# Optimization experiments

Hardware: AMD Instinct MI355X
Metric: run time of the kernel (lower is better)

## Reference

```python
import jax, jax.numpy as jnp
import numpy as np

N, E, G, H, NF, EF, GF, L = 204800, 600000, 3200, 128, 16, 5, 8, 6
EPS = 1e-5


def setup_inputs() -> dict:
    key = jax.random.key(0)
    ks = jax.random.split(key, 24)
    s = 0.05
    inp = {
        'x': jax.random.normal(ks[0], (N, NF), jnp.float32),
        'edge_index': jax.random.randint(ks[1], (2, E), 0, N, jnp.int32),
        'edge_attr': jax.random.normal(ks[2], (E, EF), jnp.float32),
        'global_features': jax.random.normal(ks[3], (G, GF), jnp.float32),
        'batch': (jnp.arange(N, dtype=jnp.int32) // (N // G)),
        'node_w': jax.random.normal(ks[4], (NF, H), jnp.float32) * s,
        'node_b': jnp.zeros((H,), jnp.float32),
        'edge_w': jax.random.normal(ks[5], (EF, H), jnp.float32) * s,
        'edge_b': jnp.zeros((H,), jnp.float32),
        'rel_w': jax.random.normal(ks[6], (L, H, H), jnp.float32) * s,
        'rel_b': jnp.zeros((L, H), jnp.float32),
        'root_w': jax.random.normal(ks[7], (L, H, H), jnp.float32) * s,
        'bn_gamma': jnp.ones((L, H), jnp.float32),
        'bn_beta': jnp.zeros((L, H), jnp.float32),
        'gate_w1': jax.random.normal(ks[8], (H, H), jnp.float32) * s,
        'gate_b1': jnp.zeros((H,), jnp.float32),
        'gate_w2': jax.random.normal(ks[9], (H, 1), jnp.float32) * s,
        'gate_b2': jnp.zeros((1,), jnp.float32),
        'gf_w': jax.random.normal(ks[10], (GF, H), jnp.float32) * s,
        'gf_b': jnp.zeros((H,), jnp.float32),
        'gi_w': jax.random.normal(ks[11], (2 * H, H), jnp.float32) * s,
        'gi_b': jnp.zeros((H,), jnp.float32),
    }
    return inp


def reference(x, edge_index, edge_attr, global_features, batch,
              node_w, node_b, edge_w, edge_b,
              rel_w, rel_b, root_w, bn_gamma, bn_beta,
              gate_w1, gate_b1, gate_w2, gate_b2,
              gf_w, gf_b, gi_w, gi_b):
    n = x.shape[0]
    src, dst = edge_index[0], edge_index[1]
    h = x @ node_w + node_b                       # [N,H]
    ea = edge_attr @ edge_w + edge_b              # [E,H]
    for i in range(L):
        identity = h
        msg = h[src] * ea                         # [E,H] gather + edge weighting
        agg = jax.ops.segment_sum(msg, dst, num_segments=n)  # scatter-add
        h2 = agg @ rel_w[i] + rel_b[i] + h @ root_w[i]        # GraphConv
        mean = jnp.mean(h2, axis=0)
        var = jnp.mean(jnp.square(h2 - mean), axis=0)         # biased (BN train)
        h2 = (h2 - mean) * jax.lax.rsqrt(var + EPS) * bn_gamma[i] + bn_beta[i]
        h = jax.nn.relu(h2 + identity)
    # GlobalAttention: segment softmax over gate scores, weighted sum of h
    gate = (jax.nn.relu(h @ gate_w1 + gate_b1) @ gate_w2 + gate_b2)[:, 0]  # [N]
    m = jax.ops.segment_max(gate, batch, num_segments=G)
    e = jnp.exp(gate - m[batch])
    ssum = jax.ops.segment_sum(e, batch, num_segments=G)
    alpha = e / ssum[batch]
    pooled = jax.ops.segment_sum(alpha[:, None] * h, batch, num_segments=G)  # [G,H]
    gf = global_features @ gf_w + gf_b
    global_embedding = jnp.concatenate([pooled, gf], axis=1) @ gi_w + gi_b
    return (h, global_embedding)
```

## Files before the change

kernel.cpp:

```cpp
#include <hip/hip_runtime.h>
#include <math.h>

#define N_NODES 204800
#define N_EDGES 600000
#define N_GRAPH 3200
#define H 128
#define NF 16
#define EF 5
#define GF 8
#define LAYERS 6
#define SEG 64
#define EPSV 1e-5f
#define NB_SCAN 800
#define NBLK 3200

typedef __attribute__((ext_vector_type(8))) short bf16x8;
typedef __attribute__((ext_vector_type(4))) float f32x4;

__device__ inline float bf2f(unsigned int u) {
    return __builtin_bit_cast(float, u << 16);
}
__device__ inline unsigned short f2bf(float f) {
    unsigned int u = __builtin_bit_cast(unsigned int, f);
    u += 0x7fffu + ((u >> 16) & 1u);
    return (unsigned short)(u >> 16);
}
__device__ inline float uif(unsigned int u) { return __builtin_bit_cast(float, u); }

__global__ __launch_bounds__(256) void k_init_h(
    const float* __restrict__ x, const float* __restrict__ node_w,
    const float* __restrict__ node_b, unsigned short* __restrict__ hb)
{
    int idx = blockIdx.x * 256 + threadIdx.x;
    int n = idx >> 5, c0 = (idx & 31) * 4;
    float4 a = *(const float4*)(node_b + c0);
    const float* xr = x + n * NF;
#pragma unroll
    for (int k = 0; k < NF; ++k) {
        float xv = xr[k];
        float4 wv = *(const float4*)(node_w + k * H + c0);
        a.x += xv * wv.x; a.y += xv * wv.y; a.z += xv * wv.z; a.w += xv * wv.w;
    }
    unsigned int p0 = (unsigned int)f2bf(a.x) | ((unsigned int)f2bf(a.y) << 16);
    unsigned int p1 = (unsigned int)f2bf(a.z) | ((unsigned int)f2bf(a.w) << 16);
    *(uint2*)(hb + (size_t)n * H + c0) = make_uint2(p0, p1);
}

__global__ __launch_bounds__(64) void k_wpack(
    const float* __restrict__ relw, const float* __restrict__ rootw,
    unsigned short* __restrict__ wp)
{
    int bid = blockIdx.x;
    int i = bid >> 6, f = bid & 63;
    int nb = f >> 3, ks = f & 7;
    int l = threadIdx.x;
    const float* src = (ks < 4) ? (relw + (size_t)i * H * H) : (rootw + (size_t)i * H * H);
    int ksl = ks & 3;
    int col = nb * 16 + (l & 15);
    int kbase = ksl * 32 + (l >> 4) * 8;
    unsigned short tmp[8];
#pragma unroll
    for (int m = 0; m < 8; ++m)
        tmp[m] = f2bf(src[(size_t)(kbase + m) * H + col]);
    *(uint4*)(wp + ((size_t)bid * 64 + l) * 8) = *(uint4*)tmp;
}

__global__ __launch_bounds__(64) void k_wpack_gate(
    const float* __restrict__ gw1, unsigned short* __restrict__ gwp)
{
    int bid = blockIdx.x;
    int nb = bid >> 2, ks = bid & 3;
    int l = threadIdx.x;
    int col = nb * 16 + (l & 15);
    int kbase = ks * 32 + (l >> 4) * 8;
    unsigned short tmp[8];
#pragma unroll
    for (int m = 0; m < 8; ++m)
        tmp[m] = f2bf(gw1[(size_t)(kbase + m) * H + col]);
    *(uint4*)(gwp + ((size_t)bid * 64 + l) * 8) = *(uint4*)tmp;
}

__global__ __launch_bounds__(256) void k_deg(const int* __restrict__ ei, int* __restrict__ deg)
{
    int e = blockIdx.x * 256 + threadIdx.x;
    if (e < N_EDGES) atomicAdd(&deg[ei[N_EDGES + e]], 1);
}

__global__ __launch_bounds__(256) void k_scan1(
    const int* __restrict__ deg, int* __restrict__ rowtmp, int* __restrict__ bsum)
{
    __shared__ int sh[256];
    int t = threadIdx.x;
    int i = blockIdx.x * 256 + t;
    int v = deg[i];
    sh[t] = v;
    __syncthreads();
    for (int off = 1; off < 256; off <<= 1) {
        int a = (t >= off) ? sh[t - off] : 0;
        __syncthreads();
        sh[t] += a;
        __syncthreads();
    }
    rowtmp[i] = sh[t] - v;
    if (t == 255) bsum[blockIdx.x] = sh[255];
}

__global__ void k_scan2(int* __restrict__ bsum, int* __restrict__ boff)
{
    __shared__ int sh[256];
    __shared__ int carry;
    int t = threadIdx.x;
    if (t == 0) carry = 0;
    __syncthreads();
    for (int base = 0; base < NB_SCAN; base += 256) {
        int i = base + t;
        int v = (i < NB_SCAN) ? bsum[i] : 0;
        sh[t] = v;
        __syncthreads();
        for (int off = 1; off < 256; off <<= 1) {
            int a = (t >= off) ? sh[t - off] : 0;
            __syncthreads();
            sh[t] += a;
            __syncthreads();
        }
        if (i < NB_SCAN) boff[i] = carry + sh[t] - v;
        __syncthreads();
        if (t == 0) carry += sh[255];
        __syncthreads();
    }
}

__global__ __launch_bounds__(256) void k_scan3(
    const int* __restrict__ rowtmp, const int* __restrict__ boff,
    int* __restrict__ rowptr, int* __restrict__ cursor)
{
    int i = blockIdx.x * 256 + threadIdx.x;
    int r = rowtmp[i] + boff[blockIdx.x];
    rowptr[i] = r;
    cursor[i] = r;
    if (i == 0) rowptr[N_NODES] = N_EDGES;
}

__global__ __launch_bounds__(256) void k_scatter(
    const int* __restrict__ ei, const float* __restrict__ eattr,
    int* __restrict__ cursor, uint4* __restrict__ recs)
{
    int e = blockIdx.x * 256 + threadIdx.x;
    if (e >= N_EDGES) return;
    int d = ei[N_EDGES + e];
    const float* ar = eattr + (size_t)e * EF;
    float c0 = ar[0], c1 = ar[1], c2 = ar[2], c3 = ar[3], c4 = ar[4];
    int pos = atomicAdd(&cursor[d], 1);
    uint4 q0, q1;
    q0.x = (unsigned int)ei[e];
    q0.y = __builtin_bit_cast(unsigned int, c0);
    q0.z = __builtin_bit_cast(unsigned int, c1);
    q0.w = __builtin_bit_cast(unsigned int, c2);
    q1.x = __builtin_bit_cast(unsigned int, c3);
    q1.y = __builtin_bit_cast(unsigned int, c4);
    q1.z = 0; q1.w = 0;
    recs[2 * (size_t)pos]     = q0;
    recs[2 * (size_t)pos + 1] = q1;
}

#define EDGE_ONE(q0, q1, A0, A1)                                               \
    {                                                                          \
        unsigned int hv = *(const unsigned int*)(hb + (size_t)(int)(q0).x * H + 2 * l); \
        float ea0 = eb2.x, ea1 = eb2.y;                                        \
        float c0 = uif((q0).y), c1 = uif((q0).z), c2 = uif((q0).w);            \
        float c3 = uif((q1).x), c4 = uif((q1).y);                              \
        ea0 += c0 * ew2[0].x + c1 * ew2[1].x + c2 * ew2[2].x + c3 * ew2[3].x + c4 * ew2[4].x; \
        ea1 += c0 * ew2[0].y + c1 * ew2[1].y + c2 * ew2[2].y + c3 * ew2[3].y + c4 * ew2[4].y; \
        A0 += bf2f(hv & 0xffffu) * ea0;                                        \
        A1 += bf2f(hv >> 16) * ea1;                                            \
    }

__global__ __launch_bounds__(256) void k_agg(
    const int* __restrict__ rowptr, const uint4* __restrict__ recs,
    const float* __restrict__ edge_w, const float* __restrict__ edge_b,
    const unsigned short* __restrict__ hb, unsigned short* __restrict__ aggb)
{
    int w = threadIdx.x >> 6, l = threadIdx.x & 63;
    int n = blockIdx.x * 8 + w * 2;
    float2 ew2[EF];
#pragma unroll
    for (int k = 0; k < EF; ++k) ew2[k] = ((const float2*)(edge_w + k * H))[l];
    float2 eb2 = ((const float2*)edge_b)[l];

    int jA = rowptr[n], eA = rowptr[n + 1];
    int jB = eA,        eB = rowptr[n + 2];
    float a0 = 0.f, a1 = 0.f, b0 = 0.f, b1 = 0.f;

    while (jA + 2 <= eA && jB + 2 <= eB) {
        uint4 qa0 = recs[2 * jA],     qa1 = recs[2 * jA + 1];
        uint4 qb0 = recs[2 * jA + 2], qb1 = recs[2 * jA + 3];
        uint4 qc0 = recs[2 * jB],     qc1 = recs[2 * jB + 1];
        uint4 qd0 = recs[2 * jB + 2], qd1 = recs[2 * jB + 3];
        EDGE_ONE(qa0, qa1, a0, a1);
        EDGE_ONE(qb0, qb1, a0, a1);
        EDGE_ONE(qc0, qc1, b0, b1);
        EDGE_ONE(qd0, qd1, b0, b1);
        jA += 2; jB += 2;
    }
    while (jA + 2 <= eA) {
        uint4 qa0 = recs[2 * jA],     qa1 = recs[2 * jA + 1];
        uint4 qb0 = recs[2 * jA + 2], qb1 = recs[2 * jA + 3];
        EDGE_ONE(qa0, qa1, a0, a1);
        EDGE_ONE(qb0, qb1, a0, a1);
        jA += 2;
    }
    if (jA < eA) {
        uint4 qa0 = recs[2 * jA], qa1 = recs[2 * jA + 1];
        EDGE_ONE(qa0, qa1, a0, a1);
    }
    while (jB + 2 <= eB) {
        uint4 qc0 = recs[2 * jB],     qc1 = recs[2 * jB + 1];
        uint4 qd0 = recs[2 * jB + 2], qd1 = recs[2 * jB + 3];
        EDGE_ONE(qc0, qc1, b0, b1);
        EDGE_ONE(qd0, qd1, b0, b1);
        jB += 2;
    }
    if (jB < eB) {
        uint4 qc0 = recs[2 * jB], qc1 = recs[2 * jB + 1];
        EDGE_ONE(qc0, qc1, b0, b1);
    }

    unsigned int pka = (unsigned int)f2bf(a0) | ((unsigned int)f2bf(a1) << 16);
    unsigned int pkb = (unsigned int)f2bf(b0) | ((unsigned int)f2bf(b1) << 16);
    *(unsigned int*)(aggb + (size_t)n * H + 2 * l)       = pka;
    *(unsigned int*)(aggb + (size_t)(n + 1) * H + 2 * l) = pkb;
}

__global__ __launch_bounds__(256) void k_gemm_mfma(
    const unsigned short* __restrict__ aggb,
    const unsigned short* __restrict__ hb,
    const unsigned short* __restrict__ wp,
    const float* __restrict__ relb,
    unsigned short* __restrict__ h2b,
    float* __restrict__ pbuf)
{
    __shared__ unsigned short smA[64 * 128];
    __shared__ unsigned short smH[64 * 128];
    int tid = threadIdx.x;
    int w = tid >> 6, l = tid & 63;
    int bid = blockIdx.x;
    int n0 = bid * 64;
    int lr = l & 15, hi = l >> 4;

    const char* aggp = (const char*)(aggb + (size_t)n0 * H);
    const char* hbp  = (const char*)(hb  + (size_t)n0 * H);
    char* sA = (char*)smA;
    char* sH = (char*)smH;
#pragma unroll
    for (int i = 0; i < 4; ++i) {
        int o = (i * 256 + tid) * 16;
        int row = o >> 8;
        int col = o & 255;
        int scol = col ^ ((row & 7) << 4);
        uint4 va = *(const uint4*)(aggp + o);
        uint4 vh = *(const uint4*)(hbp + o);
        *(uint4*)(sA + row * 256 + scol) = va;
        *(uint4*)(sH + row * 256 + scol) = vh;
    }
    __syncthreads();

    f32x4 acc[4][2];
#pragma unroll
    for (int rb = 0; rb < 4; ++rb) {
        acc[rb][0] = (f32x4){0.f, 0.f, 0.f, 0.f};
        acc[rb][1] = (f32x4){0.f, 0.f, 0.f, 0.f};
    }

    const bf16x8* wv = (const bf16x8*)wp;
#pragma unroll
    for (int ks = 0; ks < 4; ++ks) {
        bf16x8 b0 = wv[((2 * w + 0) * 8 + ks) * 64 + l];
        bf16x8 b1 = wv[((2 * w + 1) * 8 + ks) * 64 + l];
#pragma unroll
        for (int rb = 0; rb < 4; ++rb) {
            int r = rb * 16 + lr;
            int bc = (ks * 64 + hi * 16) ^ ((r & 7) << 4);
            bf16x8 a = *(const bf16x8*)(sA + r * 256 + bc);
            acc[rb][0] = __builtin_amdgcn_mfma_f32_16x16x32_bf16(a, b0, acc[rb][0], 0, 0, 0);
            acc[rb][1] = __builtin_amdgcn_mfma_f32_16x16x32_bf16(a, b1, acc[rb][1], 0, 0, 0);
        }
    }
#pragma unroll
    for (int ks = 0; ks < 4; ++ks) {
        bf16x8 b0 = wv[((2 * w + 0) * 8 + 4 + ks) * 64 + l];
        bf16x8 b1 = wv[((2 * w + 1) * 8 + 4 + ks) * 64 + l];
#pragma unroll
        for (int rb = 0; rb < 4; ++rb) {
            int r = rb * 16 + lr;
            int bc = (ks * 64 + hi * 16) ^ ((r & 7) << 4);
            bf16x8 a = *(const bf16x8*)(sH + r * 256 + bc);
            acc[rb][0] = __builtin_amdgcn_mfma_f32_16x16x32_bf16(a, b0, acc[rb][0], 0, 0, 0);
            acc[rb][1] = __builtin_amdgcn_mfma_f32_16x16x32_bf16(a, b1, acc[rb][1], 0, 0, 0);
        }
    }

#pragma unroll
    for (int nbl = 0; nbl < 2; ++nbl) {
        int col = w * 32 + nbl * 16 + lr;
        float bs = relb[col];
        float csum = 0.f, csq = 0.f;
#pragma unroll
        for (int rb = 0; rb < 4; ++rb) {
#pragma unroll
            for (int jj = 0; jj < 4; ++jj) {
                float v = acc[rb][nbl][jj] + bs;
                h2b[(size_t)(n0 + rb * 16 + hi * 4 + jj) * H + col] = f2bf(v);
                csum += v; csq += v * v;
            }
        }
        csum += __shfl_xor(csum, 16); csum += __shfl_xor(csum, 32);
        csq  += __shfl_xor(csq, 16);  csq  += __shfl_xor(csq, 32);
        if (hi == 0) {
            pbuf[(size_t)col * NBLK + bid]         = csum;
            pbuf[(size_t)(128 + col) * NBLK + bid] = csq;
        }
    }
}

__global__ __launch_bounds__(256) void k_red(
    const float* __restrict__ pbuf, const float* __restrict__ gamma,
    const float* __restrict__ beta, float* __restrict__ stats)
{
    __shared__ float sh[8];
    int c = blockIdx.x;
    int t = threadIdx.x;
    float s = 0.f, q = 0.f;
    const float* ps = pbuf + (size_t)c * NBLK;
    const float* pq = pbuf + (size_t)(128 + c) * NBLK;
    for (int i = t; i < NBLK; i += 256) { s += ps[i]; q += pq[i]; }
#pragma unroll
    for (int off = 32; off >= 1; off >>= 1) {
        s += __shfl_xor(s, off);
        q += __shfl_xor(q, off);
    }
    if ((t & 63) == 0) { sh[t >> 6] = s; sh[4 + (t >> 6)] = q; }
    __syncthreads();
    if (t == 0) {
        float S = sh[0] + sh[1] + sh[2] + sh[3];
        float Q = sh[4] + sh[5] + sh[6] + sh[7];
        float mean = S / (float)N_NODES;
        float var = fmaxf(Q / (float)N_NODES - mean * mean, 0.f);
        float scale = gamma[c] * rsqrtf(var + EPSV);
        stats[c] = scale;
        stats[128 + c] = beta[c] - mean * scale;
    }
}

template<bool LAST>
__global__ __launch_bounds__(256) void k_bn_apply(
    const unsigned short* __restrict__ h2b, const float* __restrict__ stats,
    unsigned short* __restrict__ hb, float* __restrict__ h)
{
    __shared__ float ssc[H], ssh[H];
    int tid = threadIdx.x;
    if (tid < H) {
        ssc[tid] = stats[tid];
        ssh[tid] = stats[128 + tid];
    }
    __syncthreads();
    size_t base = ((size_t)blockIdx.x * 256 + tid) * 8;
    int c = (int)(base & 127);
    uint4 hv2 = *(const uint4*)(h2b + base);
    uint4 hvp = *(const uint4*)(hb + base);
    unsigned int u2[4] = {hv2.x, hv2.y, hv2.z, hv2.w};
    unsigned int up[4] = {hvp.x, hvp.y, hvp.z, hvp.w};
    float o[8];
#pragma unroll
    for (int k = 0; k < 4; ++k) {
        float vlo = bf2f(u2[k] & 0xffffu), vhi = bf2f(u2[k] >> 16);
        float plo = bf2f(up[k] & 0xffffu), phi = bf2f(up[k] >> 16);
        o[2 * k]     = fmaxf(vlo * ssc[c + 2 * k]     + ssh[c + 2 * k]     + plo, 0.f);
        o[2 * k + 1] = fmaxf(vhi * ssc[c + 2 * k + 1] + ssh[c + 2 * k + 1] + phi, 0.f);
    }
    uint4 pk;
    pk.x = (unsigned int)f2bf(o[0]) | ((unsigned int)f2bf(o[1]) << 16);
    pk.y = (unsigned int)f2bf(o[2]) | ((unsigned int)f2bf(o[3]) << 16);
    pk.z = (unsigned int)f2bf(o[4]) | ((unsigned int)f2bf(o[5]) << 16);
    pk.w = (unsigned int)f2bf(o[6]) | ((unsigned int)f2bf(o[7]) << 16);
    *(uint4*)(hb + base) = pk;
    if (LAST) {
        *(float4*)(h + base)     = make_float4(o[0], o[1], o[2], o[3]);
        *(float4*)(h + base + 4) = make_float4(o[4], o[5], o[6], o[7]);
    }
}

__global__ __launch_bounds__(256) void k_gate_pool(
    const unsigned short* __restrict__ hb, const float* __restrict__ h,
    const unsigned short* __restrict__ gwp,
    const float* __restrict__ b1, const float* __restrict__ w2,
    const float* __restrict__ b2, float* __restrict__ pooled)
{
    __shared__ float Red[256];
    __shared__ float al[64];
    int tid = threadIdx.x;
    int w = tid >> 6, l = tid & 63;
    int lr = l & 15, hi = l >> 4;
    int g = blockIdx.x;
    int n0 = g * SEG;

    f32x4 acc[4][2];
#pragma unroll
    for (int rb = 0; rb < 4; ++rb) {
        acc[rb][0] = (f32x4){0.f, 0.f, 0.f, 0.f};
        acc[rb][1] = (f32x4){0.f, 0.f, 0.f, 0.f};
    }
    const bf16x8* wv = (const bf16x8*)gwp;
#pragma unroll
    for (int ks = 0; ks < 4; ++ks) {
        bf16x8 bb0 = wv[((2 * w + 0) * 4 + ks) * 64 + l];
        bf16x8 bb1 = wv[((2 * w + 1) * 4 + ks) * 64 + l];
#pragma unroll
        for (int rb = 0; rb < 4; ++rb) {
            bf16x8 a = *(const bf16x8*)(hb + (size_t)(n0 + rb * 16 + lr) * H + ks * 32 + hi * 8);
            acc[rb][0] = __builtin_amdgcn_mfma_f32_16x16x32_bf16(a, bb0, acc[rb][0], 0, 0, 0);
            acc[rb][1] = __builtin_amdgcn_mfma_f32_16x16x32_bf16(a, bb1, acc[rb][1], 0, 0, 0);
        }
    }
    int col0 = w * 32 + lr, col1 = w * 32 + 16 + lr;
    float b10 = b1[col0], b11 = b1[col1];
    float w20 = w2[col0], w21 = w2[col1];
    float p[4][4];
#pragma unroll
    for (int rb = 0; rb < 4; ++rb)
#pragma unroll
        for (int jj = 0; jj < 4; ++jj) {
            float v0 = fmaxf(acc[rb][0][jj] + b10, 0.f);
            float v1 = fmaxf(acc[rb][1][jj] + b11, 0.f);
            float s = v0 * w20 + v1 * w21;
            s += __shfl_xor(s, 1); s += __shfl_xor(s, 2);
            s += __shfl_xor(s, 4); s += __shfl_xor(s, 8);
            p[rb][jj] = s;
        }
    if (lr == 0) {
#pragma unroll
        for (int rb = 0; rb < 4; ++rb)
#pragma unroll
            for (int jj = 0; jj < 4; ++jj)
                Red[w * 64 + rb * 16 + hi * 4 + jj] = p[rb][jj];
    }
    __syncthreads();
    if (tid < 64) {
        float gt = Red[tid] + Red[64 + tid] + Red[128 + tid] + Red[192 + tid] + b2[0];
        float m = gt;
#pragma unroll
        for (int off = 32; off >= 1; off >>= 1) m = fmaxf(m, __shfl_xor(m, off));
        float e = expf(gt - m);
        float s = e;
#pragma unroll
        for (int off = 32; off >= 1; off >>= 1) s += __shfl_xor(s, off);
        al[tid] = e / s;
    }
    __syncthreads();
    int c = tid & 127, half = tid >> 7;
    float pp = 0.f;
    const float* hbase = h + (size_t)n0 * H;
    for (int j = half * 32; j < half * 32 + 32; ++j)
        pp += al[j] * hbase[(size_t)j * H + c];
    Red[tid] = pp;
    __syncthreads();
    if (tid < 128) pooled[(size_t)g * H + tid] = Red[tid] + Red[128 + tid];
}

__global__ __launch_bounds__(128) void k_final(
    const float* __restrict__ pooled, const float* __restrict__ gfeat,
    const float* __restrict__ gf_w, const float* __restrict__ gf_b,
    const float* __restrict__ gi_w, const float* __restrict__ gi_b,
    float* __restrict__ out)
{
    int g = blockIdx.x, c = threadIdx.x;
    __shared__ float prow[H], gfs[H];
    prow[c] = pooled[(size_t)g * H + c];
    float gv = gf_b[c];
    const float* gr = gfeat + (size_t)g * GF;
#pragma unroll
    for (int k = 0; k < GF; ++k) gv += gr[k] * gf_w[k * H + c];
    gfs[c] = gv;
    __syncthreads();
    float acc = gi_b[c];
    for (int k = 0; k < H; ++k) acc += prow[k] * gi_w[k * H + c];
    for (int k = 0; k < H; ++k) acc += gfs[k] * gi_w[(H + k) * H + c];
    out[(size_t)N_NODES * H + (size_t)g * H + c] = acc;
}

extern "C" void kernel_launch(void* const* d_in, const int* in_sizes, int n_in,
                              void* d_out, int out_size, void* d_ws, size_t ws_size,
                              hipStream_t stream)
{
    const float* x       = (const float*)d_in[0];
    const int*   ei      = (const int*)d_in[1];
    const float* eattr   = (const float*)d_in[2];
    const float* gfeat   = (const float*)d_in[3];
    const float* node_w  = (const float*)d_in[5];
    const float* node_b  = (const float*)d_in[6];
    const float* edge_w  = (const float*)d_in[7];
    const float* edge_b  = (const float*)d_in[8];
    const float* rel_w   = (const float*)d_in[9];
    const float* rel_b   = (const float*)d_in[10];
    const float* root_w  = (const float*)d_in[11];
    const float* bn_g    = (const float*)d_in[12];
    const float* bn_b    = (const float*)d_in[13];
    const float* gate_w1 = (const float*)d_in[14];
    const float* gate_b1 = (const float*)d_in[15];
    const float* gate_w2 = (const float*)d_in[16];
    const float* gate_b2 = (const float*)d_in[17];
    const float* gf_w    = (const float*)d_in[18];
    const float* gf_b    = (const float*)d_in[19];
    const float* gi_w    = (const float*)d_in[20];
    const float* gi_b    = (const float*)d_in[21];

    float* h   = (float*)d_out;
    float* out = (float*)d_out;

    char* wsb = (char*)d_ws;
    size_t off = 0;
    auto take = [&](size_t bytes) -> char* {
        char* r = wsb + off;
        off = (off + bytes + 63) & ~(size_t)63;
        return r;
    };
    unsigned short* h2b  = (unsigned short*)take((size_t)N_NODES * H * 2);
    unsigned short* hb   = (unsigned short*)take((size_t)N_NODES * H * 2);
    unsigned short* aggb = (unsigned short*)take((size_t)N_NODES * H * 2);
    unsigned short* wpck = (unsigned short*)take((size_t)LAYERS * 32768 * 2);
    unsigned short* gwp  = (unsigned short*)take((size_t)16384 * 2);
    float* pbuf   = (float*)take((size_t)256 * NBLK * 4);
    float* stats  = (float*)take((size_t)256 * 4);
    float* pooled = (float*)take((size_t)N_GRAPH * H * 4);
    int*   deg    = (int*)take((size_t)N_NODES * 4);
    int*   rowptr = (int*)take((size_t)(N_NODES + 1) * 4);
    int*   cursor = (int*)take((size_t)N_NODES * 4);
    int*   bsum   = (int*)take((size_t)NB_SCAN * 4);
    int*   boff   = (int*)take((size_t)NB_SCAN * 4);
    uint4* recs   = (uint4*)take((size_t)N_EDGES * 32);
    int*   rowtmp = cursor;

    hipMemsetAsync(deg, 0, N_NODES * sizeof(int), stream);
    k_deg<<<(N_EDGES + 255) / 256, 256, 0, stream>>>(ei, deg);
    k_scan1<<<NB_SCAN, 256, 0, stream>>>(deg, rowtmp, bsum);
    k_scan2<<<1, 256, 0, stream>>>(bsum, boff);
    k_scan3<<<NB_SCAN, 256, 0, stream>>>(rowtmp, boff, rowptr, cursor);
    k_scatter<<<(N_EDGES + 255) / 256, 256, 0, stream>>>(ei, eattr, cursor, recs);
    k_wpack<<<LAYERS * 64, 64, 0, stream>>>(rel_w, root_w, wpck);
    k_wpack_gate<<<32, 64, 0, stream>>>(gate_w1, gwp);

    k_init_h<<<N_NODES * 32 / 256, 256, 0, stream>>>(x, node_w, node_b, hb);

    for (int i = 0; i < LAYERS; ++i) {
        k_agg<<<N_NODES / 8, 256, 0, stream>>>(rowptr, recs, edge_w, edge_b, hb, aggb);
        k_gemm_mfma<<<NBLK, 256, 0, stream>>>(
            aggb, hb, wpck + (size_t)i * 32768, rel_b + (size_t)i * H,
            h2b, pbuf);
        k_red<<<128, 256, 0, stream>>>(pbuf, bn_g + (size_t)i * H, bn_b + (size_t)i * H, stats);
        if (i < LAYERS - 1)
            k_bn_apply<false><<<N_NODES * H / 8 / 256, 256, 0, stream>>>(h2b, stats, hb, h);
        else
            k_bn_apply<true><<<N_NODES * H / 8 / 256, 256, 0, stream>>>(h2b, stats, hb, h);
    }

    k_gate_pool<<<N_GRAPH, 256, 0, stream>>>(hb, h, gwp, gate_b1, gate_w2, gate_b2, pooled);
    k_final<<<N_GRAPH, H, 0, stream>>>(pooled, gfeat, gf_w, gf_b, gi_w, gi_b, out);
}
```

Before: 1.044 ms.

## Interleave four nodes per wave in aggregation with software-prefetched edge records

The aggregation kernel now has each wave process four destination nodes in lockstep instead of two. Each node's edge stream is masked so they share one loop bounded by the maximum degree, and the next edge records are loaded while the current ones are accumulated. The aim is more independent gathers in flight per wave to hide memory latency. The cost is wasted lanes of work when node degrees differ, plus extra dummy record loads at index 0. Initial embedding now has each thread compute 8 output columns with vectorized x loads and 16-byte stores.

```diff
diff --git a/kernel.cpp b/kernel.cpp
--- a/kernel.cpp
+++ b/kernel.cpp
@@ -32,18 +32,27 @@
     const float* __restrict__ node_b, unsigned short* __restrict__ hb)
 {
     int idx = blockIdx.x * 256 + threadIdx.x;
-    int n = idx >> 5, c0 = (idx & 31) * 4;
-    float4 a = *(const float4*)(node_b + c0);
-    const float* xr = x + n * NF;
+    int n = idx >> 4, c0 = (idx & 15) * 8;
+    const float4* xr = (const float4*)(x + (size_t)n * NF);
+    float4 x0 = xr[0], x1 = xr[1], x2 = xr[2], x3 = xr[3];
+    float xa[16] = {x0.x, x0.y, x0.z, x0.w, x1.x, x1.y, x1.z, x1.w,
+                    x2.x, x2.y, x2.z, x2.w, x3.x, x3.y, x3.z, x3.w};
+    float4 a0 = *(const float4*)(node_b + c0);
+    float4 a1 = *(const float4*)(node_b + c0 + 4);
 #pragma unroll
     for (int k = 0; k < NF; ++k) {
-        float xv = xr[k];
-        float4 wv = *(const float4*)(node_w + k * H + c0);
-        a.x += xv * wv.x; a.y += xv * wv.y; a.z += xv * wv.z; a.w += xv * wv.w;
-    }
-    unsigned int p0 = (unsigned int)f2bf(a.x) | ((unsigned int)f2bf(a.y) << 16);
-    unsigned int p1 = (unsigned int)f2bf(a.z) | ((unsigned int)f2bf(a.w) << 16);
-    *(uint2*)(hb + (size_t)n * H + c0) = make_uint2(p0, p1);
+        float xv = xa[k];
+        float4 w0 = *(const float4*)(node_w + k * H + c0);
+        float4 w1 = *(const float4*)(node_w + k * H + c0 + 4);
+        a0.x += xv * w0.x; a0.y += xv * w0.y; a0.z += xv * w0.z; a0.w += xv * w0.w;
+        a1.x += xv * w1.x; a1.y += xv * w1.y; a1.z += xv * w1.z; a1.w += xv * w1.w;
+    }
+    uint4 pk;
+    pk.x = (unsigned int)f2bf(a0.x) | ((unsigned int)f2bf(a0.y) << 16);
+    pk.y = (unsigned int)f2bf(a0.z) | ((unsigned int)f2bf(a0.w) << 16);
+    pk.z = (unsigned int)f2bf(a1.x) | ((unsigned int)f2bf(a1.y) << 16);
+    pk.w = (unsigned int)f2bf(a1.z) | ((unsigned int)f2bf(a1.w) << 16);
+    *(uint4*)(hb + (size_t)n * H + c0) = pk;
 }
 
 __global__ __launch_bounds__(64) void k_wpack(
@@ -163,16 +172,17 @@
     recs[2 * (size_t)pos + 1] = q1;
 }
 
-#define EDGE_ONE(q0, q1, A0, A1)                                               \
+#define EDGE_C(q0, q1, hv, vmask, A0, A1)                                      \
     {                                                                          \
-        unsigned int hv = *(const unsigned int*)(hb + (size_t)(int)(q0).x * H + 2 * l); \
         float ea0 = eb2.x, ea1 = eb2.y;                                        \
         float c0 = uif((q0).y), c1 = uif((q0).z), c2 = uif((q0).w);            \
         float c3 = uif((q1).x), c4 = uif((q1).y);                              \
         ea0 += c0 * ew2[0].x + c1 * ew2[1].x + c2 * ew2[2].x + c3 * ew2[3].x + c4 * ew2[4].x; \
         ea1 += c0 * ew2[0].y + c1 * ew2[1].y + c2 * ew2[2].y + c3 * ew2[3].y + c4 * ew2[4].y; \
-        A0 += bf2f(hv & 0xffffu) * ea0;                                        \
-        A1 += bf2f(hv >> 16) * ea1;                                            \
+        ea0 = (vmask) ? ea0 : 0.f;                                             \
+        ea1 = (vmask) ? ea1 : 0.f;                                             \
+        A0 += bf2f((hv) & 0xffffu) * ea0;                                      \
+        A1 += bf2f((hv) >> 16) * ea1;                                          \
     }
 
 __global__ __launch_bounds__(256) void k_agg(
@@ -181,54 +191,61 @@
     const unsigned short* __restrict__ hb, unsigned short* __restrict__ aggb)
 {
     int w = threadIdx.x >> 6, l = threadIdx.x & 63;
-    int n = blockIdx.x * 8 + w * 2;
+    int n = blockIdx.x * 16 + w * 4;
     float2 ew2[EF];
 #pragma unroll
     for (int k = 0; k < EF; ++k) ew2[k] = ((const float2*)(edge_w + k * H))[l];
     float2 eb2 = ((const float2*)edge_b)[l];
 
-    int jA = rowptr[n], eA = rowptr[n + 1];
-    int jB = eA,        eB = rowptr[n + 2];
-    float a0 = 0.f, a1 = 0.f, b0 = 0.f, b1 = 0.f;
-
-    while (jA + 2 <= eA && jB + 2 <= eB) {
-        uint4 qa0 = recs[2 * jA],     qa1 = recs[2 * jA + 1];
-        uint4 qb0 = recs[2 * jA + 2], qb1 = recs[2 * jA + 3];
-        uint4 qc0 = recs[2 * jB],     qc1 = recs[2 * jB + 1];
-        uint4 qd0 = recs[2 * jB + 2], qd1 = recs[2 * jB + 3];
-        EDGE_ONE(qa0, qa1, a0, a1);
-        EDGE_ONE(qb0, qb1, a0, a1);
-        EDGE_ONE(qc0, qc1, b0, b1);
-        EDGE_ONE(qd0, qd1, b0, b1);
-        jA += 2; jB += 2;
-    }
-    while (jA + 2 <= eA) {
-        uint4 qa0 = recs[2 * jA],     qa1 = recs[2 * jA + 1];
-        uint4 qb0 = recs[2 * jA + 2], qb1 = recs[2 * jA + 3];
-        EDGE_ONE(qa0, qa1, a0, a1);
-        EDGE_ONE(qb0, qb1, a0, a1);
-        jA += 2;
-    }
-    if (jA < eA) {
-        uint4 qa0 = recs[2 * jA], qa1 = recs[2 * jA + 1];
-        EDGE_ONE(qa0, qa1, a0, a1);
-    }
-    while (jB + 2 <= eB) {
-        uint4 qc0 = recs[2 * jB],     qc1 = recs[2 * jB + 1];
-        uint4 qd0 = recs[2 * jB + 2], qd1 = recs[2 * jB + 3];
-        EDGE_ONE(qc0, qc1, b0, b1);
-        EDGE_ONE(qd0, qd1, b0, b1);
-        jB += 2;
-    }
-    if (jB < eB) {
-        uint4 qc0 = recs[2 * jB], qc1 = recs[2 * jB + 1];
-        EDGE_ONE(qc0, qc1, b0, b1);
-    }
-
-    unsigned int pka = (unsigned int)f2bf(a0) | ((unsigned int)f2bf(a1) << 16);
-    unsigned int pkb = (unsigned int)f2bf(b0) | ((unsigned int)f2bf(b1) << 16);
-    *(unsigned int*)(aggb + (size_t)n * H + 2 * l)       = pka;
-    *(unsigned int*)(aggb + (size_t)(n + 1) * H + 2 * l) = pkb;
+    int j0 = rowptr[n],     e0 = rowptr[n + 1];
+    int j1 = e0,            e1 = rowptr[n + 2];
+    int j2 = e1,            e2 = rowptr[n + 3];
+    int j3 = e2,            e3 = rowptr[n + 4];
+    int iters = max(max(e0 - j0, e1 - j1), max(e2 - j2, e3 - j3));
+
+    float a00 = 0.f, a01 = 0.f, a10 = 0.f, a11 = 0.f;
+    float a20 = 0.f, a21 = 0.f, a30 = 0.f, a31 = 0.f;
+
+    int i0 = (j0 < e0) ? j0 : 0;
+    int i1 = (j1 < e1) ? j1 : 0;
+    int i2 = (j2 < e2) ? j2 : 0;
+    int i3 = (j3 < e3) ? j3 : 0;
+    uint4 qa0 = recs[2 * i0], qa1 = recs[2 * i0 + 1];
+    uint4 qb0 = recs[2 * i1], qb1 = recs[2 * i1 + 1];
+    uint4 qc0 = recs[2 * i2], qc1 = recs[2 * i2 + 1];
+    uint4 qd0 = recs[2 * i3], qd1 = recs[2 * i3 + 1];
+
+    for (int it = 0; it < iters; ++it) {
+        unsigned int hva = *(const unsigned int*)(hb + (size_t)(int)qa0.x * H + 2 * l);
+        unsigned int hvb = *(const unsigned int*)(hb + (size_t)(int)qb0.x * H + 2 * l);
+        unsigned int hvc = *(const unsigned int*)(hb + (size_t)(int)qc0.x * H + 2 * l);
+        unsigned int hvd = *(const unsigned int*)(hb + (size_t)(int)qd0.x * H + 2 * l);
+        bool v0 = j0 < e0, v1 = j1 < e1, v2 = j2 < e2, v3 = j3 < e3;
+        ++j0; ++j1; ++j2; ++j3;
+        i0 = (j0 < e0) ? j0 : 0;
+        i1 = (j1 < e1) ? j1 : 0;
+        i2 = (j2 < e2) ? j2 : 0;
+        i3 = (j3 < e3) ? j3 : 0;
+        uint4 na0 = recs[2 * i0], na1 = recs[2 * i0 + 1];
+        uint4 nb0 = recs[2 * i1], nb1 = recs[2 * i1 + 1];
+        uint4 nc0 = recs[2 * i2], nc1 = recs[2 * i2 + 1];
+        uint4 nd0 = recs[2 * i3], nd1 = recs[2 * i3 + 1];
+        EDGE_C(qa0, qa1, hva, v0, a00, a01);
+        EDGE_C(qb0, qb1, hvb, v1, a10, a11);
+        EDGE_C(qc0, qc1, hvc, v2, a20, a21);
+        EDGE_C(qd0, qd1, hvd, v3, a30, a31);
+        qa0 = na0; qa1 = na1; qb0 = nb0; qb1 = nb1;
+        qc0 = nc0; qc1 = nc1; qd0 = nd0; qd1 = nd1;
+    }
+
+    *(unsigned int*)(aggb + (size_t)n * H + 2 * l) =
+        (unsigned int)f2bf(a00) | ((unsigned int)f2bf(a01) << 16);
+    *(unsigned int*)(aggb + (size_t)(n + 1) * H + 2 * l) =
+        (unsigned int)f2bf(a10) | ((unsigned int)f2bf(a11) << 16);
+    *(unsigned int*)(aggb + (size_t)(n + 2) * H + 2 * l) =
+        (unsigned int)f2bf(a20) | ((unsigned int)f2bf(a21) << 16);
+    *(unsigned int*)(aggb + (size_t)(n + 3) * H + 2 * l) =
+        (unsigned int)f2bf(a30) | ((unsigned int)f2bf(a31) << 16);
 }
 
 __global__ __launch_bounds__(256) void k_gemm_mfma(
@@ -548,10 +565,10 @@
     k_wpack<<<LAYERS * 64, 64, 0, stream>>>(rel_w, root_w, wpck);
     k_wpack_gate<<<32, 64, 0, stream>>>(gate_w1, gwp);
 
-    k_init_h<<<N_NODES * 32 / 256, 256, 0, stream>>>(x, node_w, node_b, hb);
+    k_init_h<<<N_NODES * 16 / 256, 256, 0, stream>>>(x, node_w, node_b, hb);
 
     for (int i = 0; i < LAYERS; ++i) {
-        k_agg<<<N_NODES / 8, 256, 0, stream>>>(rowptr, recs, edge_w, edge_b, hb, aggb);
+        k_agg<<<N_NODES / 16, 256, 0, stream>>>(rowptr, recs, edge_w, edge_b, hb, aggb);
         k_gemm_mfma<<<NBLK, 256, 0, stream>>>(
             aggb, hb, wpck + (size_t)i * 32768, rel_b + (size_t)i * H,
             h2b, pbuf);
```

Result: slower. 1.111 ms (+6.4%).
